# Kernel tuning notes

Measured on AMD Instinct MI355X. Metric: run time of the kernel, lower is better.

Reference implementation:

```python
import jax, jax.numpy as jnp
import numpy as np

N_NODES = 65536
N_TREES = 32
LATENT = 256
EMB = 128
VOCAB = 600
LEVELS = 12


def setup_inputs() -> dict:
    key = jax.random.key(0)
    ks = jax.random.split(key, 24)
    f32 = jnp.float32

    def lin(k, fan_in, shape):
        return jax.random.normal(k, shape, dtype=f32) / np.float32(np.sqrt(fan_in))

    inp = {}
    inp["z"] = jax.random.normal(ks[0], (N_TREES, LATENT), dtype=f32)
    inp["emb_table"] = lin(ks[1], EMB, (VOCAB, EMB))
    inp["W_l2h"] = lin(ks[2], LATENT, (LATENT, LATENT))
    inp["b_l2h"] = jnp.zeros((LATENT,), f32)
    inp["W_ih"] = lin(ks[3], EMB, (4 * LATENT, EMB))
    inp["W_hh"] = lin(ks[4], LATENT, (4 * LATENT, LATENT))
    inp["b_ih"] = jnp.zeros((4 * LATENT,), f32)
    inp["b_hh"] = jnp.zeros((4 * LATENT,), f32)
    inp["W_ph1"] = lin(ks[5], LATENT, (LATENT, LATENT))
    inp["b_ph1"] = jnp.zeros((LATENT,), f32)
    inp["W_ph2"] = lin(ks[6], LATENT, (LATENT, LATENT))
    inp["b_ph2"] = jnp.zeros((LATENT,), f32)
    inp["W_gate"] = lin(ks[7], LATENT, (LATENT, LATENT))
    inp["b_gate"] = jnp.zeros((LATENT,), f32)
    inp["W_topo"] = lin(ks[8], LATENT, (LATENT, 3))
    inp["b_topo"] = jnp.zeros((3,), f32)
    inp["W_pred"] = lin(ks[9], LATENT, (LATENT, VOCAB))
    inp["b_pred"] = jnp.zeros((VOCAB,), f32)
    inp["features"] = jax.random.randint(ks[10], (N_NODES,), 0, VOCAB, dtype=jnp.int32)
    inp["node_level"] = jax.random.randint(ks[11], (N_NODES,), 0, LEVELS, dtype=jnp.int32)
    inp["parent_idx"] = jax.random.randint(ks[12], (N_NODES,), 0, N_NODES, dtype=jnp.int32)
    inp["sibling_idx"] = jax.random.randint(ks[13], (N_NODES,), 0, N_NODES, dtype=jnp.int32)
    inp["has_prev_sibling"] = jax.random.randint(ks[14], (N_NODES,), 0, 2, dtype=jnp.int32)
    inp["tree_id"] = jax.random.randint(ks[15], (N_NODES,), 0, N_TREES, dtype=jnp.int32)
    inp["is_parent"] = jax.random.randint(ks[16], (N_NODES,), 0, 2, dtype=jnp.int32)
    inp["has_sibling_lbl"] = jax.random.randint(ks[17], (N_NODES,), 0, 2, dtype=jnp.int32)
    inp["is_res"] = jax.random.randint(ks[18], (N_NODES,), 0, 2, dtype=jnp.int32)
    return inp


def _bce_logits(x, y):
    # numerically stable BCEWithLogits (per element, 'sum' applied by caller)
    return jnp.maximum(x, 0.0) - x * y + jnp.log1p(jnp.exp(-jnp.abs(x)))


def _lstm_cell(x, h, c, W_ih, W_hh, b_ih, b_hh):
    # torch.nn.LSTMCell gate order: i, f, g, o
    gates = x @ W_ih.T + b_ih + h @ W_hh.T + b_hh
    i, f, g, o = jnp.split(gates, 4, axis=-1)
    c_new = jax.nn.sigmoid(f) * c + jax.nn.sigmoid(i) * jnp.tanh(g)
    h_new = jax.nn.sigmoid(o) * jnp.tanh(c_new)
    return h_new, c_new


def reference(z, emb_table, W_l2h, b_l2h, W_ih, W_hh, b_ih, b_hh,
              W_ph1, b_ph1, W_ph2, b_ph2, W_gate, b_gate,
              W_topo, b_topo, W_pred, b_pred,
              features, node_level, parent_idx, sibling_idx,
              has_prev_sibling, tree_id, is_parent, has_sibling_lbl, is_res):
    N = features.shape[0]
    dt = z.dtype
    # iteration 0: latent2hidden seeds root states (c = zeros, USE_CELL_LSTM_OUTPUT=False)
    root_h = z @ W_l2h.T + b_l2h                                  # [B, L]
    lvl0 = (node_level == 0)
    h_state = jnp.where(lvl0[:, None], root_h[tree_id], 0.0)      # [N, L]
    c_state = jnp.zeros((N, root_h.shape[-1]), dt)
    emb = emb_table[features]                                     # [N, EMB]
    sib_valid = (has_prev_sibling > 0)[:, None]
    y_par = is_parent.astype(dt)
    y_sib = has_sibling_lbl.astype(dt)
    y_res = is_res.astype(dt)
    inv_n = 1.0 / N
    total_loss = jnp.zeros((), dt)
    for lvl in range(1, LEVELS):                                  # per-depth-level decode
        mask = (node_level == lvl)
        mf = mask.astype(dt)
        h_par = h_state[parent_idx]                               # gather parent states
        c_par = c_state[parent_idx]
        h_sib = jnp.where(sib_valid, h_state[sibling_idx], 0.0)   # gather prev-sibling state
        # PredictiveHidden: tanh(W1 p + W2 s)
        h_pred = jnp.tanh(h_par @ W_ph1 + b_ph1 + h_sib @ W_ph2 + b_ph2)
        # AddGate: parent + sigmoid(W s) * s
        h_par_upd = h_par + jax.nn.sigmoid(h_sib @ W_gate + b_gate) * h_sib
        # TreeTopologyPred: depth / width / is_res logits (fused 3-head linear)
        topo = h_pred @ W_topo + b_topo                           # [N, 3]
        bce = (_bce_logits(topo[:, 0], y_par)
               + _bce_logits(topo[:, 1], y_sib)
               + _bce_logits(topo[:, 2], y_res))
        total_loss = total_loss + (bce * mf).sum() * inv_n
        # label prediction: CrossEntropy(sum) / node count
        logits = h_pred @ W_pred + b_pred                         # [N, VOCAB]
        logp = jax.nn.log_softmax(logits, axis=-1)
        ce = -jnp.take_along_axis(logp, features[:, None], axis=1)[:, 0]
        total_loss = total_loss + (ce * mf).sum() * inv_n
        # tree LSTM cell update, scatter back for this level's nodes
        h_new, c_new = _lstm_cell(emb, h_par_upd, c_par, W_ih, W_hh, b_ih, b_hh)
        h_state = jnp.where(mask[:, None], h_new, h_state)
        c_state = jnp.where(mask[:, None], c_new, c_state)
    return total_loss
```

## Files before the change

### kernel.cpp

```cpp
#include <hip/hip_runtime.h>
#include <math.h>

#define LATENT 256
#define EMBD 128
#define VOCAB 600
#define NLEV 12
#define NNODES 65536
#define NTREES 32
#define MAXM 6400
#define INV_N (1.0f/65536.0f)

typedef unsigned short ushort_t;
typedef __attribute__((ext_vector_type(8))) short short8;
typedef __attribute__((ext_vector_type(4))) float float4v;
typedef __attribute__((ext_vector_type(2))) float float2v;
typedef __attribute__((ext_vector_type(8))) unsigned short u16x8;
typedef __attribute__((ext_vector_type(4))) unsigned short u16x4;

#define GLOBAL_AS __attribute__((address_space(1)))
#define LDS_AS __attribute__((address_space(3)))

__device__ __forceinline__ float sigm(float x){ return 1.0f/(1.0f+expf(-x)); }
__device__ __forceinline__ float bcef(float x, float y){
  return fmaxf(x,0.0f) - x*y + log1pf(expf(-fabsf(x)));
}
__device__ __forceinline__ ushort_t f2bf(float f){
  union{float f; unsigned u;} v; v.f=f;
  unsigned r = v.u + 0x7fffu + ((v.u>>16)&1u);
  return (ushort_t)(r>>16);
}
__device__ __forceinline__ float bf2f(ushort_t u){
  union{unsigned u; float f;} v; v.u = ((unsigned)u)<<16; return v.f;
}

__device__ __forceinline__ void gload_lds(const void* src, void* dst){
  __builtin_amdgcn_global_load_lds((const GLOBAL_AS void*)src, (LDS_AS void*)dst, 16, 0, 0);
}

__device__ __forceinline__ void acc_zero4(float4v acc[4][4]){
  #pragma unroll
  for (int i=0;i<4;i++){
    #pragma unroll
    for (int j=0;j<4;j++){ acc[i][j] = (float4v){0.f,0.f,0.f,0.f}; }
  }
}
__device__ __forceinline__ void acc_zero42(float4v acc[4][2]){
  #pragma unroll
  for (int i=0;i<4;i++){
    #pragma unroll
    for (int j=0;j<2;j++){ acc[i][j] = (float4v){0.f,0.f,0.f,0.f}; }
  }
}

__device__ __forceinline__ void stageB128(const char* Wb, int strideB, int n0, int k0,
    int srow, int skb, char* BsB, int t){
  #pragma unroll
  for (int i=0;i<4;i++){
    int row = srow + 32*i;
    int kbs = skb ^ ((row&7)<<4);
    const char* src = Wb + (size_t)(n0+row)*strideB + k0*2 + kbs;
    gload_lds(src, BsB + i*4096 + t*16);
  }
}
__device__ __forceinline__ void stageA128(const char* Ab, int strideA, int m0, int k0,
    int srow, int skb, char* AsB, int t){
  #pragma unroll
  for (int i=0;i<4;i++){
    int row = srow + 32*i;
    int kbs = skb ^ ((row&7)<<4);
    const char* src = Ab + (size_t)(m0+row)*strideA + k0*2 + kbs;
    gload_lds(src, AsB + i*4096 + t*16);
  }
}
__device__ __forceinline__ void stageA64(const char* Ab, int strideA, int m0, int k0,
    int srow, int skb, char* AsB, int t){
  #pragma unroll
  for (int i=0;i<2;i++){
    int row = srow + 32*i;
    int kbs = skb ^ ((row&7)<<4);
    const char* src = Ab + (size_t)(m0+row)*strideA + k0*2 + kbs;
    gload_lds(src, AsB + i*4096 + t*16);
  }
}

__device__ __forceinline__ void mfma_phase4(const char* AsB, const char* BsB,
    float4v acc[4][4], int lane, int wr, int wc){
  #pragma unroll
  for (int kk=0;kk<2;kk++){
    short8 af[4], bfr[4];
    const int kb = kk*64 + (lane>>4)*16;
    #pragma unroll
    for (int mf=0;mf<4;mf++){
      int row = wr*64 + mf*16 + (lane&15);
      af[mf] = *(const short8*)(AsB + row*128 + (kb ^ ((row&7)<<4)));
    }
    #pragma unroll
    for (int nf=0;nf<4;nf++){
      int row = wc*64 + nf*16 + (lane&15);
      bfr[nf] = *(const short8*)(BsB + row*128 + (kb ^ ((row&7)<<4)));
    }
    #pragma unroll
    for (int mf=0;mf<4;mf++){
      #pragma unroll
      for (int nf=0;nf<4;nf++){
        acc[mf][nf] = __builtin_amdgcn_mfma_f32_16x16x32_bf16(af[mf], bfr[nf], acc[mf][nf], 0,0,0);
      }
    }
  }
}
__device__ __forceinline__ void mfma64(const char* AsB, const char* BsB,
    float4v acc[4][2], int lane, int wv){
  #pragma unroll
  for (int kk=0;kk<2;kk++){
    short8 af[4], bfr[2];
    const int kb = kk*64 + (lane>>4)*16;
    #pragma unroll
    for (int mf=0;mf<4;mf++){
      int row = mf*16 + (lane&15);
      af[mf] = *(const short8*)(AsB + row*128 + (kb ^ ((row&7)<<4)));
    }
    #pragma unroll
    for (int nf=0;nf<2;nf++){
      int row = wv*32 + nf*16 + (lane&15);
      bfr[nf] = *(const short8*)(BsB + row*128 + (kb ^ ((row&7)<<4)));
    }
    #pragma unroll
    for (int mf=0;mf<4;mf++){
      #pragma unroll
      for (int nf=0;nf<2;nf++){
        acc[mf][nf] = __builtin_amdgcn_mfma_f32_16x16x32_bf16(af[mf], bfr[nf], acc[mf][nf], 0,0,0);
      }
    }
  }
}

__device__ __forceinline__ void epi_store_bf4(ushort_t* C, int N, int m0, int n0,
    int lane, int wr, int wc, float4v acc[4][4]){
  #pragma unroll
  for (int mf=0;mf<4;mf++){
    int rbase = m0 + wr*64 + mf*16 + (lane>>4)*4;
    #pragma unroll
    for (int nf=0;nf<4;nf++){
      int col = n0 + wc*64 + nf*16 + (lane&15);
      #pragma unroll
      for (int r=0;r<4;r++){
        C[(size_t)(rbase+r)*N + col] = f2bf(acc[mf][nf][r]);
      }
    }
  }
}
__device__ __forceinline__ void epi_store64(ushort_t* C, int N, int m0, int n0,
    int lane, int wv, float4v acc[4][2]){
  #pragma unroll
  for (int mf=0;mf<4;mf++){
    int rbase = m0 + mf*16 + (lane>>4)*4;
    #pragma unroll
    for (int nf=0;nf<2;nf++){
      int col = n0 + wv*32 + nf*16 + (lane&15);
      #pragma unroll
      for (int r=0;r<4;r++){
        C[(size_t)(rbase+r)*N + col] = f2bf(acc[mf][nf][r]);
      }
    }
  }
}

__global__ void zero_kernel(float* loss, int* counts, float* zpage){
  int t = threadIdx.x;
  if (t==0) *loss = 0.0f;
  if (t<NLEV) counts[t]=0;
  zpage[t] = 0.0f;
}

__global__ void prep_kernel(const float* __restrict__ W_ph1, const float* __restrict__ W_ph2,
    const float* __restrict__ W_gate, const float* __restrict__ W_topo,
    const float* __restrict__ W_pred, const float* __restrict__ W_ih,
    const float* __restrict__ W_hh, const float* __restrict__ emb_table,
    ushort_t* __restrict__ W1t, ushort_t* __restrict__ W2t,
    ushort_t* __restrict__ W3hh, ushort_t* __restrict__ W3ih,
    ushort_t* __restrict__ embbf)
{
  int idx = blockIdx.x*256 + threadIdx.x;
  if (idx < 512*512){
    int o = idx >> 9, k = idx & 511;
    float v;
    if (o < 256) v = (k<256) ? W_ph1[k*256+o] : W_ph2[(k-256)*256+o];
    else         v = (k<256) ? 0.0f : W_gate[(k-256)*256+(o-256)];
    W1t[idx] = f2bf(v);
    return;
  }
  idx -= 512*512;
  if (idx < 640*256){
    int o = idx >> 8, k = idx & 255;
    float v = 0.0f;
    if (o < 3) v = W_topo[k*3+o];
    else if (o >= 8 && o < 608) v = W_pred[k*VOCAB + (o-8)];
    W2t[idx] = f2bf(v);
    return;
  }
  idx -= 640*256;
  if (idx < 1024*256){
    int r = idx >> 8, k = idx & 255;
    int orig = (r&3)*256 + (r>>2);
    W3hh[idx] = f2bf(W_hh[orig*256+k]);
    return;
  }
  idx -= 1024*256;
  if (idx < 1024*128){
    int r = idx >> 7, k = idx & 127;
    int orig = (r&3)*256 + (r>>2);
    W3ih[idx] = f2bf(W_ih[orig*128+k]);
    return;
  }
  idx -= 1024*128;
  if (idx < 640*128){
    int r = idx >> 7, k = idx & 127;
    embbf[idx] = (r < VOCAB) ? f2bf(emb_table[r*EMBD+k]) : (ushort_t)0;
  }
}

__global__ __launch_bounds__(256) void eg_gemm(
    const ushort_t* __restrict__ embbf, const ushort_t* __restrict__ W3ih,
    ushort_t* __restrict__ EG)
{
  const int m0 = blockIdx.x * 128;
  const int n0 = blockIdx.y * 128;
  __shared__ ushort_t As[128*64];
  __shared__ ushort_t Bs[128*64];
  char* AsB = (char*)As; char* BsB = (char*)Bs;
  const int t = threadIdx.x, lane = t&63, wv = t>>6, wr = wv>>1, wc = wv&1;
  const int srow = t>>3, skb = (t&7)*16;
  float4v acc[4][4];
  acc_zero4(acc);
  for (int k0 = 0; k0 < 128; k0 += 64){
    stageA128((const char*)embbf, 256, m0, k0, srow, skb, AsB, t);
    stageB128((const char*)W3ih, 256, n0, k0, srow, skb, BsB, t);
    __syncthreads();
    mfma_phase4(AsB, BsB, acc, lane, wr, wc);
    __syncthreads();
  }
  epi_store_bf4(EG, 1024, m0, n0, lane, wr, wc, acc);
}

__global__ __launch_bounds__(LATENT) void root_kernel(const float* __restrict__ z,
    const float* __restrict__ W, const float* __restrict__ b, float* __restrict__ root_h){
  __shared__ float zs[LATENT];
  int bi = blockIdx.x; int t = threadIdx.x;
  zs[t] = z[bi*LATENT+t];
  __syncthreads();
  float acc = b[t];
  for (int k=0;k<LATENT;k++) acc += zs[k]*W[t*LATENT+k];
  root_h[bi*LATENT+t] = acc;
}

__global__ __launch_bounds__(LATENT) void init_kernel(const int* __restrict__ node_level,
    const int* __restrict__ tree_id, const float* __restrict__ root_h,
    ushort_t* __restrict__ h_state, ushort_t* __restrict__ c_state){
  int t = threadIdx.x;
  for (int n = blockIdx.x; n < NNODES; n += gridDim.x){
    int lvl = node_level[n];
    ushort_t h = 0;
    if (lvl==0) h = f2bf(root_h[tree_id[n]*LATENT + t]);
    h_state[(size_t)n*LATENT+t]=h;
    c_state[(size_t)n*LATENT+t]=0;
  }
}

__global__ __launch_bounds__(256) void build_lists_kernel(const int* __restrict__ node_level,
    int* __restrict__ counts, int* __restrict__ lists){
  __shared__ int lcnt[NLEV];
  __shared__ int lbase[NLEV];
  int tt = threadIdx.x;
  int n = blockIdx.x*256 + tt;
  if (tt < NLEV) lcnt[tt] = 0;
  __syncthreads();
  int lvl = node_level[n];
  int pos = atomicAdd(&lcnt[lvl], 1);
  __syncthreads();
  if (tt < NLEV) lbase[tt] = atomicAdd(&counts[tt], lcnt[tt]);
  __syncthreads();
  if (lvl >= 1){
    int p = lbase[lvl] + pos;
    if (p < MAXM) lists[lvl*MAXM + p] = n;
  }
}

__global__ __launch_bounds__(256) void k1_gemm(
    const int* __restrict__ counts, int lvl, const int* __restrict__ lists,
    const int* __restrict__ parent_idx, const int* __restrict__ sibling_idx,
    const int* __restrict__ has_prev, const ushort_t* __restrict__ h_state,
    const char* __restrict__ zpage, const ushort_t* __restrict__ W1t,
    ushort_t* __restrict__ C1, ushort_t* __restrict__ Cpb)
{
  const int count = min(counts[lvl], MAXM);
  const int m0 = blockIdx.x * 64;
  if (m0 >= count) return;
  const int y = blockIdx.y;
  const bool useHP = (y < 2);
  const int wk0 = useHP ? 0 : 256;
  const int orow0 = (y < 4) ? (y&1)*128 : 256 + (y-4)*128;
  __shared__ ushort_t As[64*64];
  __shared__ ushort_t Bs[128*64];
  char* AsB = (char*)As; char* BsB = (char*)Bs;
  const int t = threadIdx.x, lane = t&63, wv = t>>6;
  const int srow = t>>3, skb = (t&7)*16;

  const char* ab[2]; int kbs[2];
  #pragma unroll
  for (int i=0;i<2;i++){
    int row = srow + 32*i;
    kbs[i] = skb ^ ((row&7)<<4);
    int m = m0 + row;
    if (m < count){
      int node = lists[lvl*MAXM + m];
      if (useHP){
        ab[i] = (const char*)(h_state + (size_t)parent_idx[node]*LATENT);
      } else {
        ab[i] = (has_prev[node] > 0) ? (const char*)(h_state + (size_t)sibling_idx[node]*LATENT)
                                     : zpage;
      }
    } else { ab[i] = zpage; }
  }

  float4v acc[4][2];
  acc_zero42(acc);

  for (int k0 = 0; k0 < 256; k0 += 64){
    #pragma unroll
    for (int i=0;i<2;i++){
      gload_lds(ab[i] + k0*2 + kbs[i], AsB + i*4096 + t*16);
    }
    stageB128((const char*)W1t, 1024, orow0, wk0 + k0, srow, skb, BsB, t);
    __syncthreads();
    mfma64(AsB, BsB, acc, lane, wv);
    __syncthreads();
  }
  if (y >= 2 && y < 4) epi_store64(Cpb, 256, m0, orow0, lane, wv, acc);
  else                 epi_store64(C1, 512, m0, orow0, lane, wv, acc);
}

__global__ __launch_bounds__(256) void mid_kernel(
    const int* __restrict__ counts, int lvl, const int* __restrict__ lists,
    const int* __restrict__ parent_idx, const int* __restrict__ sibling_idx,
    const int* __restrict__ has_prev, const ushort_t* __restrict__ h_state,
    const ushort_t* __restrict__ c_state, const ushort_t* __restrict__ C1,
    const ushort_t* __restrict__ Cpb,
    const float* __restrict__ b_ph1, const float* __restrict__ b_ph2,
    const float* __restrict__ b_gate,
    ushort_t* __restrict__ A2, ushort_t* __restrict__ PU, ushort_t* __restrict__ Cpar)
{
  const int count = min(counts[lvl], MAXM);
  const int Mt = (count+127)&~127;
  const int t = threadIdx.x;
  const float bp = b_ph1[t] + b_ph2[t];
  const float bg = b_gate[t];
  for (int m = blockIdx.x; m < Mt; m += gridDim.x){
    if (m < count){
      int node = lists[lvl*MAXM + m];
      int pi = parent_idx[node];
      float hp = bf2f(h_state[(size_t)pi*LATENT + t]);
      float hs = (has_prev[node] > 0) ? bf2f(h_state[(size_t)sibling_idx[node]*LATENT + t]) : 0.0f;
      float pre  = bf2f(C1[(size_t)m*512 + t]) + bf2f(Cpb[(size_t)m*256 + t]) + bp;
      float gpre = bf2f(C1[(size_t)m*512 + 256 + t]) + bg;
      A2[(size_t)m*LATENT + t] = f2bf(tanhf(pre));
      PU[(size_t)m*LATENT + t] = f2bf(hp + sigm(gpre)*hs);
      Cpar[(size_t)m*LATENT + t] = c_state[(size_t)pi*LATENT + t];
    } else {
      A2[(size_t)m*LATENT + t] = 0;
      PU[(size_t)m*LATENT + t] = 0;
    }
  }
}

__global__ __launch_bounds__(256) void k2_gemm3(
    const int* __restrict__ counts, int lvl,
    const ushort_t* __restrict__ PU, const ushort_t* __restrict__ W3hh,
    ushort_t* __restrict__ C3)
{
  const int count = min(counts[lvl], MAXM);
  const int id = blockIdx.x;
  __shared__ ushort_t As[64*64];
  __shared__ ushort_t Bs[128*64];
  char* AsB = (char*)As; char* BsB = (char*)Bs;
  const int t = threadIdx.x, lane = t&63, wv = t>>6;
  const int srow = t>>3, skb = (t&7)*16;
  const int m0 = (id>>3)*64; if (m0 >= count) return;
  const int n0 = (id&7)*128;
  float4v acc[4][2];
  acc_zero42(acc);
  for (int k0 = 0; k0 < 256; k0 += 64){
    stageA64((const char*)PU, 512, m0, k0, srow, skb, AsB, t);
    stageB128((const char*)W3hh, 512, n0, k0, srow, skb, BsB, t);
    __syncthreads();
    mfma64(AsB, BsB, acc, lane, wv);
    __syncthreads();
  }
  epi_store64(C3, 1024, m0, n0, lane, wv, acc);
}

__global__ __launch_bounds__(256) void k3_lstm(
    const int* __restrict__ counts, int lvl, const int* __restrict__ lists,
    const ushort_t* __restrict__ C3,
    const ushort_t* __restrict__ Cpar, const ushort_t* __restrict__ EG,
    const float* __restrict__ b_ih, const float* __restrict__ b_hh,
    const int* __restrict__ features,
    ushort_t* __restrict__ h_state, ushort_t* __restrict__ c_state)
{
  const int count = min(counts[lvl], MAXM);
  const int t = threadIdx.x;
  const float bi = b_ih[t]       + b_hh[t];
  const float bf = b_ih[256+t]   + b_hh[256+t];
  const float bg = b_ih[512+t]   + b_hh[512+t];
  const float bo = b_ih[768+t]   + b_hh[768+t];
  for (int m = (int)blockIdx.x; m < count; m += gridDim.x){
    int node = lists[lvl*MAXM + m];
    int feat = features[node];
    u16x4 gv = *(const u16x4*)(C3 + (size_t)m*1024 + 4*t);
    u16x4 ev = *(const u16x4*)(EG + (size_t)feat*1024 + 4*t);
    float i_ = sigm(bf2f(gv[0]) + bf2f(ev[0]) + bi);
    float f_ = sigm(bf2f(gv[1]) + bf2f(ev[1]) + bf);
    float gg = tanhf(bf2f(gv[2]) + bf2f(ev[2]) + bg);
    float o_ = sigm(bf2f(gv[3]) + bf2f(ev[3]) + bo);
    float cn = f_*bf2f(Cpar[(size_t)m*LATENT+t]) + i_*gg;
    float hn = o_*tanhf(cn);
    h_state[(size_t)node*LATENT+t] = f2bf(hn);
    c_state[(size_t)node*LATENT+t] = f2bf(cn);
  }
}

__global__ __launch_bounds__(256) void loss_gemm(
    const int* __restrict__ counts, const int* __restrict__ lists,
    const int* __restrict__ features,
    const ushort_t* __restrict__ A2all, const ushort_t* __restrict__ W2t,
    const float* __restrict__ b_pred,
    float2v* __restrict__ LSEp, float* __restrict__ Lf, float* __restrict__ TopoB)
{
  const int lvl = blockIdx.y + 1;
  const int count = min(counts[lvl], MAXM);
  const int id = blockIdx.x;
  const ushort_t* A2 = A2all + (size_t)lvl*MAXM*LATENT;
  float2v* LSEl = LSEp + (size_t)lvl*MAXM*5;
  float* Lfl = Lf + (size_t)lvl*MAXM;
  float* Topol = TopoB + (size_t)lvl*MAXM*3;
  __shared__ ushort_t SMEM[2*128*64];
  char* AsB = (char*)SMEM;
  char* BsB = (char*)(SMEM + 128*64);
  float* lse_lds = (float*)SMEM;
  int* sh_feat = (int*)((char*)SMEM + 4096);
  const int t = threadIdx.x, lane = t&63, wv = t>>6, wr = wv>>1, wc = wv&1;
  const int srow = t>>3, skb = (t&7)*16;

  const int m0 = (id/5)*128; if (m0 >= count) return;
  const int nblk = id%5;
  const int n0 = nblk*128;
  float4v acc[4][4];
  acc_zero4(acc);
  for (int k0 = 0; k0 < 256; k0 += 64){
    stageA128((const char*)A2, 512, m0, k0, srow, skb, AsB, t);
    stageB128((const char*)W2t, 512, n0, k0, srow, skb, BsB, t);
    __syncthreads();
    mfma_phase4(AsB, BsB, acc, lane, wr, wc);
    __syncthreads();
  }
  if (t < 128){
    int m = m0 + t;
    sh_feat[t] = (m < count) ? (features[lists[lvl*MAXM + m]] + 8) : -9999;
  }
  __syncthreads();
  int colv[4]; bool valid[4]; float bias[4];
  #pragma unroll
  for (int nf=0;nf<4;nf++){
    colv[nf] = n0 + wc*64 + nf*16 + (lane&15);
    valid[nf] = (colv[nf] >= 8 && colv[nf] < 608);
    bias[nf] = valid[nf] ? b_pred[colv[nf]-8] : 0.0f;
  }
  #pragma unroll
  for (int mf=0;mf<4;mf++){
    #pragma unroll
    for (int r=0;r<4;r++){
      int row = wr*64 + mf*16 + (lane>>4)*4 + r;
      float v[4];
      #pragma unroll
      for (int nf=0;nf<4;nf++){
        float raw = acc[mf][nf][r];
        float val = raw + bias[nf];
        if (colv[nf] == sh_feat[row]) Lfl[m0+row] = val;
        if (nblk==0 && colv[nf] < 3) Topol[(size_t)(m0+row)*3 + colv[nf]] = raw;
        v[nf] = valid[nf] ? val : -1e30f;
      }
      float mx = fmaxf(fmaxf(v[0],v[1]), fmaxf(v[2],v[3]));
      #pragma unroll
      for (int off=8;off>=1;off>>=1) mx = fmaxf(mx, __shfl_xor(mx, off));
      float s = expf(v[0]-mx)+expf(v[1]-mx)+expf(v[2]-mx)+expf(v[3]-mx);
      #pragma unroll
      for (int off=8;off>=1;off>>=1) s += __shfl_xor(s, off);
      if ((lane&15)==0){
        lse_lds[row*4 + wc*2 + 0] = mx;
        lse_lds[row*4 + wc*2 + 1] = s;
      }
    }
  }
  __syncthreads();
  if (t < 128){
    float M = fmaxf(lse_lds[t*4+0], lse_lds[t*4+2]);
    float S = lse_lds[t*4+1]*expf(lse_lds[t*4+0]-M)
            + lse_lds[t*4+3]*expf(lse_lds[t*4+2]-M);
    LSEl[(size_t)(m0+t)*5 + nblk] = (float2v){M, S};
  }
}

__global__ __launch_bounds__(256) void loss_merge(
    const int* __restrict__ counts, const int* __restrict__ lists,
    const float2v* __restrict__ LSEp, const float* __restrict__ Lf,
    const float* __restrict__ TopoB,
    const float* __restrict__ b_topo,
    const int* __restrict__ is_parent, const int* __restrict__ has_sib,
    const int* __restrict__ is_res,
    float* __restrict__ loss)
{
  const int lvl = blockIdx.y + 1;
  const int count = min(counts[lvl], MAXM);
  const float2v* LSEl = LSEp + (size_t)lvl*MAXM*5;
  const float* Lfl = Lf + (size_t)lvl*MAXM;
  const float* Topol = TopoB + (size_t)lvl*MAXM*3;
  __shared__ float lsum[4];
  const int wvi = threadIdx.x >> 6;
  if (threadIdx.x < 4) lsum[threadIdx.x] = 0.0f;
  __syncthreads();
  float acc = 0.0f;
  const float bt0 = b_topo[0], bt1 = b_topo[1], bt2 = b_topo[2];
  for (int m = blockIdx.x*256 + threadIdx.x; m < count; m += 8192){
    int node = lists[lvl*MAXM + m];
    float M = -1e30f;
    float2v p[5];
    #pragma unroll
    for (int b=0;b<5;b++){ p[b] = LSEl[(size_t)m*5 + b]; M = fmaxf(M, p[b][0]); }
    float S = 0.0f;
    #pragma unroll
    for (int b=0;b<5;b++) S += p[b][1] * expf(p[b][0] - M);
    float ce = logf(S) + M - Lfl[m];
    float bce = bcef(Topol[(size_t)m*3+0]+bt0, (float)is_parent[node])
              + bcef(Topol[(size_t)m*3+1]+bt1, (float)has_sib[node])
              + bcef(Topol[(size_t)m*3+2]+bt2, (float)is_res[node]);
    acc += ce + bce;
  }
  #pragma unroll
  for (int off=32;off>=1;off>>=1) acc += __shfl_xor(acc, off);
  if ((threadIdx.x&63)==0) atomicAdd(&lsum[wvi], acc);
  __syncthreads();
  if (threadIdx.x == 0){
    atomicAdd(loss, (lsum[0]+lsum[1]+lsum[2]+lsum[3]) * INV_N);
  }
}

extern "C" void kernel_launch(void* const* d_in, const int* in_sizes, int n_in,
                              void* d_out, int out_size, void* d_ws, size_t ws_size,
                              hipStream_t stream)
{
  const float* z         = (const float*)d_in[0];
  const float* emb_table = (const float*)d_in[1];
  const float* W_l2h     = (const float*)d_in[2];
  const float* b_l2h     = (const float*)d_in[3];
  const float* W_ih      = (const float*)d_in[4];
  const float* W_hh      = (const float*)d_in[5];
  const float* b_ih      = (const float*)d_in[6];
  const float* b_hh      = (const float*)d_in[7];
  const float* W_ph1     = (const float*)d_in[8];
  const float* b_ph1     = (const float*)d_in[9];
  const float* W_ph2     = (const float*)d_in[10];
  const float* b_ph2     = (const float*)d_in[11];
  const float* W_gate    = (const float*)d_in[12];
  const float* b_gate    = (const float*)d_in[13];
  const float* W_topo    = (const float*)d_in[14];
  const float* b_topo    = (const float*)d_in[15];
  const float* W_pred    = (const float*)d_in[16];
  const float* b_pred    = (const float*)d_in[17];
  const int* features    = (const int*)d_in[18];
  const int* node_level  = (const int*)d_in[19];
  const int* parent_idx  = (const int*)d_in[20];
  const int* sibling_idx = (const int*)d_in[21];
  const int* has_prev    = (const int*)d_in[22];
  const int* tree_id     = (const int*)d_in[23];
  const int* is_parent   = (const int*)d_in[24];
  const int* has_sib     = (const int*)d_in[25];
  const int* is_res      = (const int*)d_in[26];

  char* ws = (char*)d_ws;
  size_t off = 0;
  auto alloc = [&](size_t bytes)->char*{
    char* p = ws + off; off += (bytes + 255) & ~(size_t)255; return p;
  };
  ushort_t* h_state = (ushort_t*)alloc((size_t)NNODES*LATENT*2);
  ushort_t* c_state = (ushort_t*)alloc((size_t)NNODES*LATENT*2);
  ushort_t* A2all   = (ushort_t*)alloc((size_t)NLEV*MAXM*LATENT*2);
  ushort_t* PU      = (ushort_t*)alloc((size_t)MAXM*LATENT*2);
  ushort_t* C1      = (ushort_t*)alloc((size_t)MAXM*512*2);
  ushort_t* Cpb     = (ushort_t*)alloc((size_t)MAXM*256*2);
  ushort_t* C3      = (ushort_t*)alloc((size_t)MAXM*1024*2);
  ushort_t* Cpar    = (ushort_t*)alloc((size_t)MAXM*LATENT*2);
  float2v*  LSEp    = (float2v*)alloc((size_t)NLEV*MAXM*5*8);
  float*    Lf      = (float*)alloc((size_t)NLEV*MAXM*4);
  float*    TopoB   = (float*)alloc((size_t)NLEV*MAXM*3*4);
  ushort_t* W1t     = (ushort_t*)alloc((size_t)512*512*2);
  ushort_t* W2t     = (ushort_t*)alloc((size_t)640*256*2);
  ushort_t* W3hh    = (ushort_t*)alloc((size_t)1024*256*2);
  ushort_t* W3ih    = (ushort_t*)alloc((size_t)1024*128*2);
  ushort_t* embbf   = (ushort_t*)alloc((size_t)640*128*2);
  ushort_t* EG      = (ushort_t*)alloc((size_t)640*1024*2);
  float*    root_h  = (float*)alloc((size_t)NTREES*LATENT*4);
  int*      lists   = (int*)alloc((size_t)NLEV*MAXM*4);
  int*      counts  = (int*)alloc(64);
  float*    zpage   = (float*)alloc(1024);
  float*    loss    = (float*)d_out;

  zero_kernel<<<1,256,0,stream>>>(loss, counts, zpage);
  prep_kernel<<<3520,256,0,stream>>>(W_ph1,W_ph2,W_gate,W_topo,W_pred,W_ih,W_hh,emb_table,
                                     W1t,W2t,W3hh,W3ih,embbf);
  eg_gemm<<<dim3(5,8),256,0,stream>>>(embbf, W3ih, EG);
  root_kernel<<<NTREES,LATENT,0,stream>>>(z, W_l2h, b_l2h, root_h);
  init_kernel<<<2048,LATENT,0,stream>>>(node_level, tree_id, root_h, h_state, c_state);
  build_lists_kernel<<<NNODES/256,256,0,stream>>>(node_level, counts, lists);

  for (int lvl=1; lvl<NLEV; lvl++){
    ushort_t* A2 = A2all + (size_t)lvl*MAXM*LATENT;
    k1_gemm<<<dim3(MAXM/64,6),256,0,stream>>>(counts, lvl, lists,
        parent_idx, sibling_idx, has_prev, h_state, (const char*)zpage, W1t, C1, Cpb);
    mid_kernel<<<2048,256,0,stream>>>(counts, lvl, lists, parent_idx, sibling_idx,
        has_prev, h_state, c_state, C1, Cpb, b_ph1, b_ph2, b_gate, A2, PU, Cpar);
    k2_gemm3<<<800,256,0,stream>>>(counts, lvl, PU, W3hh, C3);
    k3_lstm<<<2048,256,0,stream>>>(counts, lvl, lists, C3, Cpar, EG,
        b_ih, b_hh, features, h_state, c_state);
  }

  loss_gemm<<<dim3(250,NLEV-1),256,0,stream>>>(counts, lists, features,
      A2all, W2t, b_pred, LSEp, Lf, TopoB);
  loss_merge<<<dim3(32,NLEV-1),256,0,stream>>>(counts, lists, LSEp, Lf, TopoB,
      b_topo, is_parent, has_sib, is_res, loss);
}
```

Before: 486.4 us.

## Keep A tile resident in LDS and sweep all vocab chunks per block

```diff
diff --git a/kernel.cpp b/kernel.cpp
--- a/kernel.cpp
+++ b/kernel.cpp
@@ -433,85 +433,104 @@
     const int* __restrict__ features,
     const ushort_t* __restrict__ A2all, const ushort_t* __restrict__ W2t,
     const float* __restrict__ b_pred,
-    float2v* __restrict__ LSEp, float* __restrict__ Lf, float* __restrict__ TopoB)
+    float2v* __restrict__ LSE, float* __restrict__ Lf, float* __restrict__ TopoB)
 {
   const int lvl = blockIdx.y + 1;
   const int count = min(counts[lvl], MAXM);
-  const int id = blockIdx.x;
+  const int m0 = blockIdx.x * 128;
+  if (m0 >= count) return;
   const ushort_t* A2 = A2all + (size_t)lvl*MAXM*LATENT;
-  float2v* LSEl = LSEp + (size_t)lvl*MAXM*5;
+  float2v* LSEl = LSE + (size_t)lvl*MAXM;
   float* Lfl = Lf + (size_t)lvl*MAXM;
   float* Topol = TopoB + (size_t)lvl*MAXM*3;
-  __shared__ ushort_t SMEM[2*128*64];
-  char* AsB = (char*)SMEM;
-  char* BsB = (char*)(SMEM + 128*64);
-  float* lse_lds = (float*)SMEM;
-  int* sh_feat = (int*)((char*)SMEM + 4096);
+  __shared__ ushort_t As[4*128*64];
+  __shared__ ushort_t Bs[128*64];
+  char* AsB = (char*)As; char* BsB = (char*)Bs;
   const int t = threadIdx.x, lane = t&63, wv = t>>6, wr = wv>>1, wc = wv&1;
   const int srow = t>>3, skb = (t&7)*16;
 
-  const int m0 = (id/5)*128; if (m0 >= count) return;
-  const int nblk = id%5;
-  const int n0 = nblk*128;
-  float4v acc[4][4];
-  acc_zero4(acc);
-  for (int k0 = 0; k0 < 256; k0 += 64){
-    stageA128((const char*)A2, 512, m0, k0, srow, skb, AsB, t);
-    stageB128((const char*)W2t, 512, n0, k0, srow, skb, BsB, t);
-    __syncthreads();
-    mfma_phase4(AsB, BsB, acc, lane, wr, wc);
-    __syncthreads();
-  }
+  #pragma unroll
+  for (int c=0;c<4;c++){
+    stageA128((const char*)A2, 512, m0, c*64, srow, skb, AsB + c*16384, t);
+  }
+  int featr[16];
+  #pragma unroll
+  for (int j=0;j<16;j++){
+    int row = wr*64 + (j>>2)*16 + (lane>>4)*4 + (j&3);
+    int m = m0 + row;
+    featr[j] = (m < count) ? (features[lists[lvl*MAXM + m]] + 8) : -9999;
+  }
+  float runM[16], runS[16];
+  #pragma unroll
+  for (int j=0;j<16;j++){ runM[j] = -1e30f; runS[j] = 0.0f; }
+
+  for (int nchunk=0; nchunk<5; nchunk++){
+    const int n0 = nchunk*128;
+    float4v acc[4][4];
+    acc_zero4(acc);
+    #pragma unroll
+    for (int c=0;c<4;c++){
+      stageB128((const char*)W2t, 512, n0, c*64, srow, skb, BsB, t);
+      __syncthreads();
+      mfma_phase4(AsB + c*16384, BsB, acc, lane, wr, wc);
+      __syncthreads();
+    }
+    int colv[4]; bool valid[4]; float bias[4];
+    #pragma unroll
+    for (int nf=0;nf<4;nf++){
+      colv[nf] = n0 + wc*64 + nf*16 + (lane&15);
+      valid[nf] = (colv[nf] >= 8 && colv[nf] < 608);
+      bias[nf] = valid[nf] ? b_pred[colv[nf]-8] : 0.0f;
+    }
+    #pragma unroll
+    for (int mf=0;mf<4;mf++){
+      #pragma unroll
+      for (int r=0;r<4;r++){
+        int j = mf*4 + r;
+        int row = wr*64 + mf*16 + (lane>>4)*4 + r;
+        float v[4];
+        #pragma unroll
+        for (int nf=0;nf<4;nf++){
+          float raw = acc[mf][nf][r];
+          float val = raw + bias[nf];
+          if (colv[nf] == featr[j]) Lfl[m0+row] = val;
+          if (nchunk==0 && colv[nf] < 3) Topol[(size_t)(m0+row)*3 + colv[nf]] = raw;
+          v[nf] = valid[nf] ? val : -1e30f;
+        }
+        float mx = fmaxf(fmaxf(v[0],v[1]), fmaxf(v[2],v[3]));
+        #pragma unroll
+        for (int off=8;off>=1;off>>=1) mx = fmaxf(mx, __shfl_xor(mx, off));
+        float s = expf(v[0]-mx)+expf(v[1]-mx)+expf(v[2]-mx)+expf(v[3]-mx);
+        #pragma unroll
+        for (int off=8;off>=1;off>>=1) s += __shfl_xor(s, off);
+        float nM = fmaxf(runM[j], mx);
+        runS[j] = runS[j]*expf(runM[j]-nM) + s*expf(mx-nM);
+        runM[j] = nM;
+      }
+    }
+  }
+  __syncthreads();
+  float* scr = (float*)Bs;
+  if ((lane&15)==0){
+    #pragma unroll
+    for (int j=0;j<16;j++){
+      int row = wr*64 + (j>>2)*16 + (lane>>4)*4 + (j&3);
+      scr[row*4 + wc*2 + 0] = runM[j];
+      scr[row*4 + wc*2 + 1] = runS[j];
+    }
+  }
+  __syncthreads();
   if (t < 128){
-    int m = m0 + t;
-    sh_feat[t] = (m < count) ? (features[lists[lvl*MAXM + m]] + 8) : -9999;
-  }
-  __syncthreads();
-  int colv[4]; bool valid[4]; float bias[4];
-  #pragma unroll
-  for (int nf=0;nf<4;nf++){
-    colv[nf] = n0 + wc*64 + nf*16 + (lane&15);
-    valid[nf] = (colv[nf] >= 8 && colv[nf] < 608);
-    bias[nf] = valid[nf] ? b_pred[colv[nf]-8] : 0.0f;
-  }
-  #pragma unroll
-  for (int mf=0;mf<4;mf++){
-    #pragma unroll
-    for (int r=0;r<4;r++){
-      int row = wr*64 + mf*16 + (lane>>4)*4 + r;
-      float v[4];
-      #pragma unroll
-      for (int nf=0;nf<4;nf++){
-        float raw = acc[mf][nf][r];
-        float val = raw + bias[nf];
-        if (colv[nf] == sh_feat[row]) Lfl[m0+row] = val;
-        if (nblk==0 && colv[nf] < 3) Topol[(size_t)(m0+row)*3 + colv[nf]] = raw;
-        v[nf] = valid[nf] ? val : -1e30f;
-      }
-      float mx = fmaxf(fmaxf(v[0],v[1]), fmaxf(v[2],v[3]));
-      #pragma unroll
-      for (int off=8;off>=1;off>>=1) mx = fmaxf(mx, __shfl_xor(mx, off));
-      float s = expf(v[0]-mx)+expf(v[1]-mx)+expf(v[2]-mx)+expf(v[3]-mx);
-      #pragma unroll
-      for (int off=8;off>=1;off>>=1) s += __shfl_xor(s, off);
-      if ((lane&15)==0){
-        lse_lds[row*4 + wc*2 + 0] = mx;
-        lse_lds[row*4 + wc*2 + 1] = s;
-      }
-    }
-  }
-  __syncthreads();
-  if (t < 128){
-    float M = fmaxf(lse_lds[t*4+0], lse_lds[t*4+2]);
-    float S = lse_lds[t*4+1]*expf(lse_lds[t*4+0]-M)
-            + lse_lds[t*4+3]*expf(lse_lds[t*4+2]-M);
-    LSEl[(size_t)(m0+t)*5 + nblk] = (float2v){M, S};
+    float M = fmaxf(scr[t*4+0], scr[t*4+2]);
+    float S = scr[t*4+1]*expf(scr[t*4+0]-M)
+            + scr[t*4+3]*expf(scr[t*4+2]-M);
+    LSEl[m0+t] = (float2v){M, S};
   }
 }
 
 __global__ __launch_bounds__(256) void loss_merge(
     const int* __restrict__ counts, const int* __restrict__ lists,
-    const float2v* __restrict__ LSEp, const float* __restrict__ Lf,
+    const float2v* __restrict__ LSE, const float* __restrict__ Lf,
     const float* __restrict__ TopoB,
     const float* __restrict__ b_topo,
     const int* __restrict__ is_parent, const int* __restrict__ has_sib,
@@ -520,7 +539,7 @@
 {
   const int lvl = blockIdx.y + 1;
   const int count = min(counts[lvl], MAXM);
-  const float2v* LSEl = LSEp + (size_t)lvl*MAXM*5;
+  const float2v* LSEl = LSE + (size_t)lvl*MAXM;
   const float* Lfl = Lf + (size_t)lvl*MAXM;
   const float* Topol = TopoB + (size_t)lvl*MAXM*3;
   __shared__ float lsum[4];
@@ -531,14 +550,8 @@
   const float bt0 = b_topo[0], bt1 = b_topo[1], bt2 = b_topo[2];
   for (int m = blockIdx.x*256 + threadIdx.x; m < count; m += 8192){
     int node = lists[lvl*MAXM + m];
-    float M = -1e30f;
-    float2v p[5];
-    #pragma unroll
-    for (int b=0;b<5;b++){ p[b] = LSEl[(size_t)m*5 + b]; M = fmaxf(M, p[b][0]); }
-    float S = 0.0f;
-    #pragma unroll
-    for (int b=0;b<5;b++) S += p[b][1] * expf(p[b][0] - M);
-    float ce = logf(S) + M - Lfl[m];
+    float2v p = LSEl[m];
+    float ce = logf(p[1]) + p[0] - Lfl[m];
     float bce = bcef(Topol[(size_t)m*3+0]+bt0, (float)is_parent[node])
               + bcef(Topol[(size_t)m*3+1]+bt1, (float)has_sib[node])
               + bcef(Topol[(size_t)m*3+2]+bt2, (float)is_res[node]);
@@ -598,7 +611,7 @@
   ushort_t* Cpb     = (ushort_t*)alloc((size_t)MAXM*256*2);
   ushort_t* C3      = (ushort_t*)alloc((size_t)MAXM*1024*2);
   ushort_t* Cpar    = (ushort_t*)alloc((size_t)MAXM*LATENT*2);
-  float2v*  LSEp    = (float2v*)alloc((size_t)NLEV*MAXM*5*8);
+  float2v*  LSE     = (float2v*)alloc((size_t)NLEV*MAXM*8);
   float*    Lf      = (float*)alloc((size_t)NLEV*MAXM*4);
   float*    TopoB   = (float*)alloc((size_t)NLEV*MAXM*3*4);
   ushort_t* W1t     = (ushort_t*)alloc((size_t)512*512*2);
@@ -632,8 +645,8 @@
         b_ih, b_hh, features, h_state, c_state);
   }
 
-  loss_gemm<<<dim3(250,NLEV-1),256,0,stream>>>(counts, lists, features,
-      A2all, W2t, b_pred, LSEp, Lf, TopoB);
-  loss_merge<<<dim3(32,NLEV-1),256,0,stream>>>(counts, lists, LSEp, Lf, TopoB,
+  loss_gemm<<<dim3(50,NLEV-1),256,0,stream>>>(counts, lists, features,
+      A2all, W2t, b_pred, LSE, Lf, TopoB);
+  loss_merge<<<dim3(32,NLEV-1),256,0,stream>>>(counts, lists, LSE, Lf, TopoB,
       b_topo, is_parent, has_sib, is_res, loss);
 }
```

After: 550.7 us. 1.13x slower.
